# Performance work log

Hardware: AMD Instinct MI355X
Metric: run time of the kernel (lower is better)

The kernel has to match this reference:

```python
import jax, jax.numpy as jnp
import numpy as np

N_NODES = 50000
N_EDGES = 800000
IN_CH = 128
HID = 128   # 2 * out_channels
OUT = 64
LN_EPS = 1e-5
L2_EPS = 1e-12


def setup_inputs() -> dict:
    key = jax.random.key(0)
    ks = jax.random.split(key, 12)
    x = jax.random.normal(ks[0], (N_NODES, IN_CH), dtype=jnp.float32)
    edge_index = jax.random.randint(ks[1], (2, N_EDGES), 0, N_NODES, dtype=jnp.int64)
    # GCNConv weights (glorot-ish scale) + bias; LayerNorm gamma/beta
    W1 = jax.random.normal(ks[2], (IN_CH, HID), dtype=jnp.float32) * (1.0 / np.sqrt(IN_CH))
    b1 = jnp.zeros((HID,), dtype=jnp.float32)
    g1 = jnp.ones((HID,), dtype=jnp.float32)
    beta1 = jnp.zeros((HID,), dtype=jnp.float32)
    W2 = jax.random.normal(ks[3], (HID, OUT), dtype=jnp.float32) * (1.0 / np.sqrt(HID))
    b2 = jnp.zeros((OUT,), dtype=jnp.float32)
    g2 = jnp.ones((OUT,), dtype=jnp.float32)
    beta2 = jnp.zeros((OUT,), dtype=jnp.float32)
    return {"x": x, "edge_index": edge_index, "W1": W1, "b1": b1, "g1": g1,
            "beta1": beta1, "W2": W2, "b2": b2, "g2": g2, "beta2": beta2}


def _layer_norm(h, gamma, beta):
    mu = jnp.mean(h, axis=-1, keepdims=True)
    var = jnp.mean(jnp.square(h - mu), axis=-1, keepdims=True)
    return (h - mu) * jax.lax.rsqrt(var + LN_EPS) * gamma + beta


def reference(x, edge_index, W1, b1, g1, beta1, W2, b2, g2, beta2):
    # Add self-loops once; compute symmetric GCN normalization (shared by both layers).
    loops = jnp.arange(N_NODES, dtype=edge_index.dtype)
    src = jnp.concatenate([edge_index[0], loops])  # [E+N]
    dst = jnp.concatenate([edge_index[1], loops])  # [E+N]
    deg = jax.ops.segment_sum(jnp.ones_like(dst, dtype=x.dtype), dst,
                              num_segments=N_NODES)
    dinv = jnp.where(deg > 0, jax.lax.rsqrt(deg), 0.0)
    norm = dinv[src] * dinv[dst]  # [E+N]

    def gcn_conv(h, W, b):
        h = h @ W                                   # [N, d_out]
        msg = h[src] * norm[:, None]                # gather + scale  [E+N, d_out]
        agg = jax.ops.segment_sum(msg, dst, num_segments=N_NODES)
        return agg + b

    h = jax.nn.relu(_layer_norm(gcn_conv(x, W1, b1), g1, beta1))
    # Dropout(0.4) is identity in eval mode (correctness baseline).
    h = jax.nn.relu(_layer_norm(gcn_conv(h, W2, b2), g2, beta2))
    nrm = jnp.sqrt(jnp.sum(jnp.square(h), axis=1, keepdims=True))
    return h / jnp.maximum(nrm, L2_EPS)
```

## Files before the change

kernel.cpp:

```cpp
#include <hip/hip_runtime.h>
#include <hip/hip_fp16.h>


#define K_DIM 128

typedef _Float16 f16x8 __attribute__((ext_vector_type(8)));
typedef _Float16 f16x4 __attribute__((ext_vector_type(4)));
typedef float f32x4 __attribute__((ext_vector_type(4)));

__global__ __launch_bounds__(256) void hist_kernel(const int* __restrict__ dst,
                                                   int* counts, int E) {
    int i = blockIdx.x * 256 + threadIdx.x;
    if (i < E) atomicAdd(&counts[dst[i]], 1);
}

__global__ __launch_bounds__(256) void scan_block_kernel(const int* __restrict__ counts,
                                                         int* row_ptr, int* partials,
                                                         float* dinv, int N) {
    __shared__ int sm[256];
    int t = threadIdx.x;
    int i = blockIdx.x * 256 + t;
    int v = (i < N) ? counts[i] : 0;
    if (i < N) dinv[i] = rsqrtf((float)(v + 1));
    sm[t] = v;
    __syncthreads();
    for (int off = 1; off < 256; off <<= 1) {
        int add = (t >= off) ? sm[t - off] : 0;
        __syncthreads();
        sm[t] += add;
        __syncthreads();
    }
    if (i < N) row_ptr[i] = sm[t] - v;
    if (t == 255) partials[blockIdx.x] = sm[255];
}

__global__ __launch_bounds__(256) void scan_partials_kernel(int* partials, int NB) {
    __shared__ int sm[256];
    int t = threadIdx.x;
    int v = (t < NB) ? partials[t] : 0;
    sm[t] = v;
    __syncthreads();
    for (int off = 1; off < 256; off <<= 1) {
        int add = (t >= off) ? sm[t - off] : 0;
        __syncthreads();
        sm[t] += add;
        __syncthreads();
    }
    if (t < NB) partials[t] = sm[t] - v;
}

__global__ __launch_bounds__(256) void fill_kernel(const int* __restrict__ src,
                                                   const int* __restrict__ dst,
                                                   const float* __restrict__ dinv,
                                                   int* row_ptr,
                                                   const int* __restrict__ partials,
                                                   int2* edges, int E) {
    int i = blockIdx.x * 256 + threadIdx.x;
    if (i < E) {
        int d = dst[i];
        int s = src[i];
        int pos = atomicAdd(&row_ptr[d], 1) + partials[d >> 8];
        edges[pos] = make_int2(s, __float_as_int(dinv[s] * dinv[d]));
    }
}

__global__ __launch_bounds__(256) void wt_prep_kernel(const float* __restrict__ W1,
                                                      _Float16* __restrict__ WT) {
    int idx = blockIdx.x * 256 + threadIdx.x;
    if (idx < 128 * 128) {
        int k = idx >> 7, j = idx & 127;
        WT[j * 128 + k] = (_Float16)W1[idx];
    }
}

__global__ __launch_bounds__(256) void gemm1_mfma_kernel(const float* __restrict__ X,
                                                         const _Float16* __restrict__ WT,
                                                         __half* __restrict__ H, int N) {
    __shared__ _Float16 As[64][136];

    int row0 = blockIdx.x * 64;
    {
        int r = threadIdx.x >> 2;
        int c0 = (threadIdx.x & 3) * 32;
        int row = row0 + r;
        if (row < N) {
            const float4* srcp = (const float4*)(X + (size_t)row * 128 + c0);
#pragma unroll
            for (int i = 0; i < 8; ++i) {
                float4 v = srcp[i];
                f16x4 h = {(_Float16)v.x, (_Float16)v.y, (_Float16)v.z, (_Float16)v.w};
                *(f16x4*)&As[r][c0 + 4 * i] = h;
            }
        } else {
            f16x4 z = {};
#pragma unroll
            for (int i = 0; i < 8; ++i) *(f16x4*)&As[r][c0 + 4 * i] = z;
        }
    }
    __syncthreads();

    int wave = threadIdx.x >> 6;
    int lane = threadIdx.x & 63;
    int l15 = lane & 15;
    int k0 = (lane >> 4) * 8;
    int arow = wave * 16 + l15;

    f32x4 acc[8] = {};
#pragma unroll
    for (int ks = 0; ks < 4; ++ks) {
        f16x8 a = *(const f16x8*)&As[arow][ks * 32 + k0];
#pragma unroll
        for (int t = 0; t < 8; ++t) {
            f16x8 b = *(const f16x8*)(WT + (size_t)(t * 16 + l15) * 128 + ks * 32 + k0);
            acc[t] = __builtin_amdgcn_mfma_f32_16x16x32_f16(a, b, acc[t], 0, 0, 0);
        }
    }

    int rbase = row0 + wave * 16 + (lane >> 4) * 4;
#pragma unroll
    for (int t = 0; t < 8; ++t) {
#pragma unroll
        for (int r = 0; r < 4; ++r) {
            int row = rbase + r;
            if (row < N) H[(size_t)row * 128 + t * 16 + l15] = __float2half(acc[t][r]);
        }
    }
}

__global__ __launch_bounds__(256) void gather1_fused_kernel(
    const __half* __restrict__ h1, const float* __restrict__ dinv,
    const int* __restrict__ row_ptr, const int* __restrict__ counts,
    const int* __restrict__ partials, const int2* __restrict__ edges,
    const float* __restrict__ b1, const float* __restrict__ g1,
    const float* __restrict__ beta1, const float* __restrict__ W2,
    __half* __restrict__ h3, int N) {
    __shared__ float lds[4][K_DIM];
    int wave = threadIdx.x >> 6;
    int lane = threadIdx.x & 63;
    int node = blockIdx.x * 4 + wave;
    if (node >= N) return;

    float dd = dinv[node];
    float2 acc = __half22float2(((const __half2*)(h1 + (size_t)node * 128))[lane]);
    acc.x *= dd * dd; acc.y *= dd * dd;

    int end = row_ptr[node] + partials[node >> 8];
    int beg = end - counts[node];
    int e = beg;
    for (; e + 8 <= end; e += 8) {
        int2 rc[8];
#pragma unroll
        for (int i = 0; i < 8; ++i) rc[i] = edges[e + i];
        __half2 v[8];
#pragma unroll
        for (int i = 0; i < 8; ++i)
            v[i] = ((const __half2*)(h1 + (size_t)rc[i].x * 128))[lane];
#pragma unroll
        for (int i = 0; i < 8; ++i) {
            float w = __int_as_float(rc[i].y);
            float2 f = __half22float2(v[i]);
            acc.x = fmaf(f.x, w, acc.x);
            acc.y = fmaf(f.y, w, acc.y);
        }
    }
    for (; e + 4 <= end; e += 4) {
        int2 rc[4];
#pragma unroll
        for (int i = 0; i < 4; ++i) rc[i] = edges[e + i];
        __half2 v[4];
#pragma unroll
        for (int i = 0; i < 4; ++i)
            v[i] = ((const __half2*)(h1 + (size_t)rc[i].x * 128))[lane];
#pragma unroll
        for (int i = 0; i < 4; ++i) {
            float w = __int_as_float(rc[i].y);
            float2 f = __half22float2(v[i]);
            acc.x = fmaf(f.x, w, acc.x);
            acc.y = fmaf(f.y, w, acc.y);
        }
    }
    for (; e < end; ++e) {
        int2 rc = edges[e];
        float w = __int_as_float(rc.y);
        float2 f = __half22float2(((const __half2*)(h1 + (size_t)rc.x * 128))[lane]);
        acc.x = fmaf(f.x, w, acc.x);
        acc.y = fmaf(f.y, w, acc.y);
    }

    float2 bb = ((const float2*)b1)[lane];
    acc.x += bb.x; acc.y += bb.y;
    float s = acc.x + acc.y;
    for (int off = 32; off; off >>= 1) s += __shfl_xor(s, off);
    float mu = s * (1.0f / 128.0f);
    float dx = acc.x - mu, dy = acc.y - mu;
    float q = dx * dx + dy * dy;
    for (int off = 32; off; off >>= 1) q += __shfl_xor(q, off);
    float rstd = rsqrtf(q * (1.0f / 128.0f) + 1e-5f);
    float2 gg = ((const float2*)g1)[lane];
    float2 be = ((const float2*)beta1)[lane];
    float ox = fmaxf(fmaf(dx * rstd, gg.x, be.x), 0.0f);
    float oy = fmaxf(fmaf(dy * rstd, gg.y, be.y), 0.0f);

    ((float2*)&lds[wave][0])[lane] = make_float2(ox, oy);
    float o = 0.0f;
#pragma unroll 8
    for (int k = 0; k < K_DIM; k += 4) {
        float4 vv = *(const float4*)&lds[wave][k];
        o = fmaf(vv.x, W2[(size_t)(k + 0) * 64 + lane], o);
        o = fmaf(vv.y, W2[(size_t)(k + 1) * 64 + lane], o);
        o = fmaf(vv.z, W2[(size_t)(k + 2) * 64 + lane], o);
        o = fmaf(vv.w, W2[(size_t)(k + 3) * 64 + lane], o);
    }
    h3[(size_t)node * 64 + lane] = __float2half(o);
}

__global__ __launch_bounds__(256) void gather2_fused_kernel(
    const __half* __restrict__ h3, const float* __restrict__ dinv,
    const int* __restrict__ row_ptr, const int* __restrict__ counts,
    const int* __restrict__ partials, const int2* __restrict__ edges,
    const float* __restrict__ b2, const float* __restrict__ g2,
    const float* __restrict__ beta2, float* __restrict__ out, int N) {
    int wave = threadIdx.x >> 6;
    int lane = threadIdx.x & 63;
    int node = blockIdx.x * 4 + wave;
    if (node >= N) return;

    float dd = dinv[node];
    float acc = __half2float(h3[(size_t)node * 64 + lane]) * dd * dd;

    int end = row_ptr[node] + partials[node >> 8];
    int beg = end - counts[node];
    int e = beg;
    for (; e + 8 <= end; e += 8) {
        int2 rc[8];
#pragma unroll
        for (int i = 0; i < 8; ++i) rc[i] = edges[e + i];
        __half v[8];
#pragma unroll
        for (int i = 0; i < 8; ++i) v[i] = h3[(size_t)rc[i].x * 64 + lane];
#pragma unroll
        for (int i = 0; i < 8; ++i)
            acc = fmaf(__half2float(v[i]), __int_as_float(rc[i].y), acc);
    }
    for (; e + 4 <= end; e += 4) {
        int2 rc[4];
#pragma unroll
        for (int i = 0; i < 4; ++i) rc[i] = edges[e + i];
        __half v[4];
#pragma unroll
        for (int i = 0; i < 4; ++i) v[i] = h3[(size_t)rc[i].x * 64 + lane];
#pragma unroll
        for (int i = 0; i < 4; ++i)
            acc = fmaf(__half2float(v[i]), __int_as_float(rc[i].y), acc);
    }
    for (; e < end; ++e) {
        int2 rc = edges[e];
        acc = fmaf(__half2float(h3[(size_t)rc.x * 64 + lane]), __int_as_float(rc.y), acc);
    }

    float v = acc + b2[lane];
    float s = v;
    for (int off = 32; off; off >>= 1) s += __shfl_xor(s, off);
    float mu = s * (1.0f / 64.0f);
    float d = v - mu;
    float q = d * d;
    for (int off = 32; off; off >>= 1) q += __shfl_xor(q, off);
    float rstd = rsqrtf(q * (1.0f / 64.0f) + 1e-5f);
    float o = fmaxf(fmaf(d * rstd, g2[lane], beta2[lane]), 0.0f);
    float q2 = o * o;
    for (int off = 32; off; off >>= 1) q2 += __shfl_xor(q2, off);
    float nrm = sqrtf(q2);
    out[(size_t)node * 64 + lane] = o / fmaxf(nrm, 1e-12f);
}

extern "C" void kernel_launch(void* const* d_in, const int* in_sizes, int n_in,
                              void* d_out, int out_size, void* d_ws, size_t ws_size,
                              hipStream_t stream) {
    const float* x     = (const float*)d_in[0];
    const int*   ei    = (const int*)d_in[1];
    const float* W1    = (const float*)d_in[2];
    const float* b1    = (const float*)d_in[3];
    const float* g1    = (const float*)d_in[4];
    const float* beta1 = (const float*)d_in[5];
    const float* W2    = (const float*)d_in[6];
    const float* b2    = (const float*)d_in[7];
    const float* g2    = (const float*)d_in[8];
    const float* beta2 = (const float*)d_in[9];

    const int N = in_sizes[0] / 128;
    const int E = in_sizes[1] / 2;
    const int* src = ei;
    const int* dst = ei + E;
    float* out = (float*)d_out;

    char* p = (char*)d_ws;
    auto alloc = [&](size_t bytes) { char* r = p; p += (bytes + 255) & ~(size_t)255; return r; };
    int*      counts   = (int*)alloc((size_t)N * 4);
    int*      row_ptr  = (int*)alloc((size_t)N * 4);
    int*      partials = (int*)alloc(256 * 4);
    float*    dinv     = (float*)alloc((size_t)N * 4);
    int2*     edges    = (int2*)alloc((size_t)E * 8);
    _Float16* WT       = (_Float16*)alloc(128 * 128 * 2);
    __half*   h1       = (__half*)alloc((size_t)N * 128 * 2);
    __half*   h3       = (__half*)alloc((size_t)N * 64 * 2);

    const int nb_nodes = (N + 255) / 256;
    const int nb_edges = (E + 255) / 256;
    const int nb_wave_nodes = (N + 3) / 4;

    hipMemsetAsync(counts, 0, (size_t)N * 4, stream);
    hist_kernel<<<nb_edges, 256, 0, stream>>>(dst, counts, E);
    scan_block_kernel<<<nb_nodes, 256, 0, stream>>>(counts, row_ptr, partials, dinv, N);
    scan_partials_kernel<<<1, 256, 0, stream>>>(partials, nb_nodes);
    fill_kernel<<<nb_edges, 256, 0, stream>>>(src, dst, dinv, row_ptr, partials, edges, E);

    wt_prep_kernel<<<64, 256, 0, stream>>>(W1, WT);
    gemm1_mfma_kernel<<<(N + 63) / 64, 256, 0, stream>>>(x, WT, h1, N);

    gather1_fused_kernel<<<nb_wave_nodes, 256, 0, stream>>>(
        h1, dinv, row_ptr, counts, partials, edges, b1, g1, beta1, W2, h3, N);

    gather2_fused_kernel<<<nb_wave_nodes, 256, 0, stream>>>(
        h3, dinv, row_ptr, counts, partials, edges, b2, g2, beta2, out, N);
}
```

Measured before the change: 224.9 us.

## Split gather-aggregation into feature-sliced edge-parallel kernels with separate LayerNorm passes

```diff
diff --git a/kernel.cpp b/kernel.cpp
--- a/kernel.cpp
+++ b/kernel.cpp
@@ -127,72 +127,79 @@
     }
 }
 
-__global__ __launch_bounds__(256) void gather1_fused_kernel(
+__global__ __launch_bounds__(256) void agg1_sliced_kernel(
     const __half* __restrict__ h1, const float* __restrict__ dinv,
     const int* __restrict__ row_ptr, const int* __restrict__ counts,
     const int* __restrict__ partials, const int2* __restrict__ edges,
-    const float* __restrict__ b1, const float* __restrict__ g1,
-    const float* __restrict__ beta1, const float* __restrict__ W2,
-    __half* __restrict__ h3, int N) {
+    float* __restrict__ agg1, int N) {
+    int slice = blockIdx.x & 3;
+    int wave = threadIdx.x >> 6;
+    int node = (blockIdx.x >> 2) * 4 + wave;
+    if (node >= N) return;
+    int lane = threadIdx.x & 63;
+    int sub = lane >> 4;
+    int cp = lane & 15;
+
+    const __half2* h2 = (const __half2*)h1;
+    int coff = slice * 16 + cp;
+
+    float2 acc = make_float2(0.0f, 0.0f);
+    if (sub == 0) {
+        float dd = dinv[node];
+        float2 f = __half22float2(h2[(size_t)node * 64 + coff]);
+        acc.x = f.x * dd * dd;
+        acc.y = f.y * dd * dd;
+    }
+
+    int end = row_ptr[node] + partials[node >> 8];
+    int beg = end - counts[node];
+    for (int e = beg; e < end; e += 16) {
+        long long rec[4];
+#pragma unroll
+        for (int u = 0; u < 4; ++u) {
+            int idx = e + 4 * u + sub;
+            int cidx = idx < end ? idx : end - 1;
+            rec[u] = __builtin_nontemporal_load((const long long*)&edges[cidx]);
+            if (idx >= end) rec[u] &= 0xFFFFFFFFLL;
+        }
+        __half2 v[4];
+#pragma unroll
+        for (int u = 0; u < 4; ++u)
+            v[u] = h2[(size_t)(int)rec[u] * 64 + coff];
+#pragma unroll
+        for (int u = 0; u < 4; ++u) {
+            float w = __int_as_float((int)(rec[u] >> 32));
+            float2 f = __half22float2(v[u]);
+            acc.x = fmaf(f.x, w, acc.x);
+            acc.y = fmaf(f.y, w, acc.y);
+        }
+    }
+
+    acc.x += __shfl_xor(acc.x, 16);
+    acc.y += __shfl_xor(acc.y, 16);
+    acc.x += __shfl_xor(acc.x, 32);
+    acc.y += __shfl_xor(acc.y, 32);
+    if (sub == 0)
+        ((float2*)(agg1 + (size_t)node * 128 + slice * 32))[cp] = acc;
+}
+
+__global__ __launch_bounds__(256) void ln1_w2_kernel(
+    const float* __restrict__ agg1, const float* __restrict__ b1,
+    const float* __restrict__ g1, const float* __restrict__ beta1,
+    const float* __restrict__ W2, __half* __restrict__ h3, int N) {
     __shared__ float lds[4][K_DIM];
     int wave = threadIdx.x >> 6;
     int lane = threadIdx.x & 63;
     int node = blockIdx.x * 4 + wave;
     if (node >= N) return;
 
-    float dd = dinv[node];
-    float2 acc = __half22float2(((const __half2*)(h1 + (size_t)node * 128))[lane]);
-    acc.x *= dd * dd; acc.y *= dd * dd;
-
-    int end = row_ptr[node] + partials[node >> 8];
-    int beg = end - counts[node];
-    int e = beg;
-    for (; e + 8 <= end; e += 8) {
-        int2 rc[8];
-#pragma unroll
-        for (int i = 0; i < 8; ++i) rc[i] = edges[e + i];
-        __half2 v[8];
-#pragma unroll
-        for (int i = 0; i < 8; ++i)
-            v[i] = ((const __half2*)(h1 + (size_t)rc[i].x * 128))[lane];
-#pragma unroll
-        for (int i = 0; i < 8; ++i) {
-            float w = __int_as_float(rc[i].y);
-            float2 f = __half22float2(v[i]);
-            acc.x = fmaf(f.x, w, acc.x);
-            acc.y = fmaf(f.y, w, acc.y);
-        }
-    }
-    for (; e + 4 <= end; e += 4) {
-        int2 rc[4];
-#pragma unroll
-        for (int i = 0; i < 4; ++i) rc[i] = edges[e + i];
-        __half2 v[4];
-#pragma unroll
-        for (int i = 0; i < 4; ++i)
-            v[i] = ((const __half2*)(h1 + (size_t)rc[i].x * 128))[lane];
-#pragma unroll
-        for (int i = 0; i < 4; ++i) {
-            float w = __int_as_float(rc[i].y);
-            float2 f = __half22float2(v[i]);
-            acc.x = fmaf(f.x, w, acc.x);
-            acc.y = fmaf(f.y, w, acc.y);
-        }
-    }
-    for (; e < end; ++e) {
-        int2 rc = edges[e];
-        float w = __int_as_float(rc.y);
-        float2 f = __half22float2(((const __half2*)(h1 + (size_t)rc.x * 128))[lane]);
-        acc.x = fmaf(f.x, w, acc.x);
-        acc.y = fmaf(f.y, w, acc.y);
-    }
-
+    float2 a = ((const float2*)(agg1 + (size_t)node * 128))[lane];
     float2 bb = ((const float2*)b1)[lane];
-    acc.x += bb.x; acc.y += bb.y;
-    float s = acc.x + acc.y;
+    a.x += bb.x; a.y += bb.y;
+    float s = a.x + a.y;
     for (int off = 32; off; off >>= 1) s += __shfl_xor(s, off);
     float mu = s * (1.0f / 128.0f);
-    float dx = acc.x - mu, dy = acc.y - mu;
+    float dx = a.x - mu, dy = a.y - mu;
     float q = dx * dx + dy * dy;
     for (int off = 32; off; off >>= 1) q += __shfl_xor(q, off);
     float rstd = rsqrtf(q * (1.0f / 128.0f) + 1e-5f);
@@ -214,51 +221,72 @@
     h3[(size_t)node * 64 + lane] = __float2half(o);
 }
 
-__global__ __launch_bounds__(256) void gather2_fused_kernel(
+__global__ __launch_bounds__(256) void agg2_sliced_kernel(
     const __half* __restrict__ h3, const float* __restrict__ dinv,
     const int* __restrict__ row_ptr, const int* __restrict__ counts,
     const int* __restrict__ partials, const int2* __restrict__ edges,
-    const float* __restrict__ b2, const float* __restrict__ g2,
-    const float* __restrict__ beta2, float* __restrict__ out, int N) {
+    float* __restrict__ agg2, int N) {
+    int slice = blockIdx.x & 1;
+    int wave = threadIdx.x >> 6;
+    int node = (blockIdx.x >> 1) * 4 + wave;
+    if (node >= N) return;
+    int lane = threadIdx.x & 63;
+    int sub = lane >> 4;
+    int cp = lane & 15;
+
+    const __half2* h2 = (const __half2*)h3;
+    int coff = slice * 16 + cp;
+
+    float2 acc = make_float2(0.0f, 0.0f);
+    if (sub == 0) {
+        float dd = dinv[node];
+        float2 f = __half22float2(h2[(size_t)node * 32 + coff]);
+        acc.x = f.x * dd * dd;
+        acc.y = f.y * dd * dd;
+    }
+
+    int end = row_ptr[node] + partials[node >> 8];
+    int beg = end - counts[node];
+    for (int e = beg; e < end; e += 16) {
+        long long rec[4];
+#pragma unroll
+        for (int u = 0; u < 4; ++u) {
+            int idx = e + 4 * u + sub;
+            int cidx = idx < end ? idx : end - 1;
+            rec[u] = __builtin_nontemporal_load((const long long*)&edges[cidx]);
+            if (idx >= end) rec[u] &= 0xFFFFFFFFLL;
+        }
+        __half2 v[4];
+#pragma unroll
+        for (int u = 0; u < 4; ++u)
+            v[u] = h2[(size_t)(int)rec[u] * 32 + coff];
+#pragma unroll
+        for (int u = 0; u < 4; ++u) {
+            float w = __int_as_float((int)(rec[u] >> 32));
+            float2 f = __half22float2(v[u]);
+            acc.x = fmaf(f.x, w, acc.x);
+            acc.y = fmaf(f.y, w, acc.y);
+        }
+    }
+
+    acc.x += __shfl_xor(acc.x, 16);
+    acc.y += __shfl_xor(acc.y, 16);
+    acc.x += __shfl_xor(acc.x, 32);
+    acc.y += __shfl_xor(acc.y, 32);
+    if (sub == 0)
+        ((float2*)(agg2 + (size_t)node * 64 + slice * 32))[cp] = acc;
+}
+
+__global__ __launch_bounds__(256) void ln2_l2_kernel(
+    const float* __restrict__ agg2, const float* __restrict__ b2,
+    const float* __restrict__ g2, const float* __restrict__ beta2,
+    float* __restrict__ out, int N) {
     int wave = threadIdx.x >> 6;
     int lane = threadIdx.x & 63;
     int node = blockIdx.x * 4 + wave;
     if (node >= N) return;
 
-    float dd = dinv[node];
-    float acc = __half2float(h3[(size_t)node * 64 + lane]) * dd * dd;
-
-    int end = row_ptr[node] + partials[node >> 8];
-    int beg = end - counts[node];
-    int e = beg;
-    for (; e + 8 <= end; e += 8) {
-        int2 rc[8];
-#pragma unroll
-        for (int i = 0; i < 8; ++i) rc[i] = edges[e + i];
-        __half v[8];
-#pragma unroll
-        for (int i = 0; i < 8; ++i) v[i] = h3[(size_t)rc[i].x * 64 + lane];
-#pragma unroll
-        for (int i = 0; i < 8; ++i)
-            acc = fmaf(__half2float(v[i]), __int_as_float(rc[i].y), acc);
-    }
-    for (; e + 4 <= end; e += 4) {
-        int2 rc[4];
-#pragma unroll
-        for (int i = 0; i < 4; ++i) rc[i] = edges[e + i];
-        __half v[4];
-#pragma unroll
-        for (int i = 0; i < 4; ++i) v[i] = h3[(size_t)rc[i].x * 64 + lane];
-#pragma unroll
-        for (int i = 0; i < 4; ++i)
-            acc = fmaf(__half2float(v[i]), __int_as_float(rc[i].y), acc);
-    }
-    for (; e < end; ++e) {
-        int2 rc = edges[e];
-        acc = fmaf(__half2float(h3[(size_t)rc.x * 64 + lane]), __int_as_float(rc.y), acc);
-    }
-
-    float v = acc + b2[lane];
+    float v = agg2[(size_t)node * 64 + lane] + b2[lane];
     float s = v;
     for (int off = 32; off; off >>= 1) s += __shfl_xor(s, off);
     float mu = s * (1.0f / 64.0f);
@@ -302,7 +330,9 @@
     int2*     edges    = (int2*)alloc((size_t)E * 8);
     _Float16* WT       = (_Float16*)alloc(128 * 128 * 2);
     __half*   h1       = (__half*)alloc((size_t)N * 128 * 2);
+    float*    agg1     = (float*)alloc((size_t)N * 128 * 4);
     __half*   h3       = (__half*)alloc((size_t)N * 64 * 2);
+    float*    agg2     = (float*)h1;
 
     const int nb_nodes = (N + 255) / 256;
     const int nb_edges = (E + 255) / 256;
@@ -317,9 +347,11 @@
     wt_prep_kernel<<<64, 256, 0, stream>>>(W1, WT);
     gemm1_mfma_kernel<<<(N + 63) / 64, 256, 0, stream>>>(x, WT, h1, N);
 
-    gather1_fused_kernel<<<nb_wave_nodes, 256, 0, stream>>>(
-        h1, dinv, row_ptr, counts, partials, edges, b1, g1, beta1, W2, h3, N);
-
-    gather2_fused_kernel<<<nb_wave_nodes, 256, 0, stream>>>(
-        h3, dinv, row_ptr, counts, partials, edges, b2, g2, beta2, out, N);
-}
+    agg1_sliced_kernel<<<nb_wave_nodes * 4, 256, 0, stream>>>(
+        h1, dinv, row_ptr, counts, partials, edges, agg1, N);
+    ln1_w2_kernel<<<nb_wave_nodes, 256, 0, stream>>>(agg1, b1, g1, beta1, W2, h3, N);
+
+    agg2_sliced_kernel<<<nb_wave_nodes * 2, 256, 0, stream>>>(
+        h3, dinv, row_ptr, counts, partials, edges, agg2, N);
+    ln2_l2_kernel<<<nb_wave_nodes, 256, 0, stream>>>(agg2, b2, g2, beta2, out, N);
+}
```

New measurement: 333.2 us. +48.1%, slower.
